# Performance work log

Measured on AMD Instinct MI355X. Metric: run time of the kernel, lower is better.

The kernel has to match this reference:

```python
import jax, jax.numpy as jnp
import numpy as np

EPS_ATTN = 1e-6
EPS_LN = 1e-5


def _layer_norm(x, g, b):
    m = jnp.mean(x, axis=-1, keepdims=True)
    v = jnp.mean((x - m) ** 2, axis=-1, keepdims=True)
    return (x - m) * jax.lax.rsqrt(v + EPS_LN) * g + b


def _linear_attention(q, k, v):
    # q,k,v: [N, L/S, H, D]; elu feature map (+1 keeps values positive)
    q = jax.nn.elu(q) + 1.0
    k = jax.nn.elu(k) + 1.0
    s_len = v.shape[1]
    v = v / s_len
    kv = jnp.einsum('nshd,nshv->nhdv', k, v)            # [N,H,D,D]
    z = 1.0 / (jnp.einsum('nlhd,nhd->nlh', q, k.sum(axis=1)) + EPS_ATTN)
    out = jnp.einsum('nlhd,nhdv->nlhv', q, kv) * z[..., None] * s_len
    return out


def setup_inputs() -> dict:
    key = jax.random.key(0)
    ks = jax.random.split(key, 8)
    N, L, S, H, D = 4, 4096, 4096, 8, 64
    sc = 0.05
    return {
        'x': jax.random.normal(ks[0], (N, L, H, D), jnp.float32),
        'source': jax.random.normal(ks[1], (N, S, H, D), jnp.float32),
        'wq': jax.random.normal(ks[2], (D, D), jnp.float32) * sc,
        'wk': jax.random.normal(ks[3], (D, D), jnp.float32) * sc,
        'wv': jax.random.normal(ks[4], (D, D), jnp.float32) * sc,
        'wmerge': jax.random.normal(ks[5], (D, D), jnp.float32) * sc,
        'w1': jax.random.normal(ks[6], (2 * D, 2 * D), jnp.float32) * sc,
        'w2': jax.random.normal(ks[7], (D, 2 * D), jnp.float32) * sc,
        'g1': jnp.ones((D,), jnp.float32),
        'b1': jnp.zeros((D,), jnp.float32),
        'g2': jnp.ones((D,), jnp.float32),
        'b2': jnp.zeros((D,), jnp.float32),
    }


def reference(x, source, wq, wk, wv, wmerge, w1, w2, g1, b1, g2, b2):
    # projections (torch Linear: y = x @ W.T), applied on last dim D=d_model
    q = jnp.einsum('nlhd,ed->nlhe', x, wq)
    k = jnp.einsum('nshd,ed->nshe', source, wk)
    v = jnp.einsum('nshd,ed->nshe', source, wv)
    message = _linear_attention(q, k, v)                # [N,L,H,D]
    message = jnp.einsum('nlhd,ed->nlhe', message, wmerge)
    message = _layer_norm(message, g1, b1)
    h = jnp.concatenate([x, message], axis=-1)          # [N,L,H,2D]
    h = jax.nn.relu(jnp.einsum('nlhd,ed->nlhe', h, w1))
    h = jnp.einsum('nlhd,ed->nlhe', h, w2)              # [N,L,H,D]
    h = _layer_norm(h, g2, b2)
    return x + h
```

## Files before the change

### kernel.cpp

```cpp
#include <hip/hip_runtime.h>
#include <cstdint>

#define NB 4
#define LL 4096
#define SS 4096
#define HH 8
#define DD 64
#define NHC (NB*HH)

typedef unsigned short ushort_t;
typedef __bf16 bf16x8 __attribute__((ext_vector_type(8)));
typedef float f32x4 __attribute__((ext_vector_type(4)));
typedef unsigned short u16x8 __attribute__((ext_vector_type(8)));

__device__ __forceinline__ float bf2f(unsigned short u) {
    union { unsigned int i; float f; } v; v.i = ((unsigned int)u) << 16; return v.f;
}
__device__ __forceinline__ unsigned short f2bf(float f) {
    union { float ff; unsigned int i; } v; v.ff = f;
    unsigned int x = v.i;
    x += 0x7fffu + ((x >> 16) & 1u);
    return (unsigned short)(x >> 16);
}
__device__ __forceinline__ bool input_is_bf16(const void* g1) {
    return ((const unsigned short*)g1)[0] == 0x3F80u;
}

template<bool BF16>
__device__ __forceinline__ float ldgf(const void* p, size_t i) {
    if constexpr (BF16) return bf2f(((const unsigned short*)p)[i]);
    else                return ((const float*)p)[i];
}
template<bool BF16>
__device__ __forceinline__ u16x8 ld8(const void* p, size_t i) {
    if constexpr (BF16) {
        return *reinterpret_cast<const u16x8*>((const unsigned short*)p + i);
    } else {
        const float* f = (const float*)p + i;
        u16x8 o;
        #pragma unroll
        for (int j = 0; j < 8; ++j) o[j] = f2bf(f[j]);
        return o;
    }
}
__device__ __forceinline__ bf16x8 ldsA(const ushort_t* p) {
    return *reinterpret_cast<const bf16x8*>(p);
}
#define MFMA16(a,b,c) __builtin_amdgcn_mfma_f32_16x16x32_bf16(a,b,c,0,0,0)

template<bool BF16, int LC>
__device__ __forceinline__ void stage_w(const void* g, size_t goff, ushort_t* dst,
                                        int rows, int dstride, int tid) {
    int total8 = (rows << LC) >> 3;
    for (int i8 = tid; i8 < total8; i8 += 256) {
        int i = i8 << 3;
        int r = i >> LC, c = i & ((1 << LC) - 1);
        *reinterpret_cast<u16x8*>(dst + r * dstride + c) = ld8<BF16>(g, goff + i);
    }
}

__device__ __forceinline__ void red16(float v[4]) {
    #pragma unroll
    for (int m = 1; m < 16; m <<= 1) {
        #pragma unroll
        for (int r = 0; r < 4; ++r) v[r] += __shfl_xor(v[r], m);
    }
}

template<bool BF16>
__device__ void kv_body(const void* __restrict__ src, const void* __restrict__ wk,
                        const void* __restrict__ wv, float* __restrict__ kvg,
                        float* __restrict__ ksumg,
                        ushort_t* S, ushort_t* KT, ushort_t* VT)
{
    const int tid = threadIdx.x;
    const int lane = tid & 63, w = tid >> 6;
    const int lg = lane >> 4, l15 = lane & 15;
    const int bid = blockIdx.x;
    const int nh = bid >> 3, ch = bid & 7;
    const int n = nh >> 3, h = nh & 7;
    const int s0 = ch * 512;
    const f32x4 z4 = {0.f, 0.f, 0.f, 0.f};

    stage_w<BF16, 6>(wk, 0, KT, 64, 136, tid);
    stage_w<BF16, 6>(wv, 0, VT, 64, 136, tid);
    __syncthreads();
    bf16x8 wkf[2][4], wvf[2][4];
    #pragma unroll
    for (int ks = 0; ks < 2; ++ks)
        #pragma unroll
        for (int nt = 0; nt < 4; ++nt) {
            wkf[ks][nt] = ldsA(KT + (nt * 16 + l15) * 136 + ks * 32 + lg * 8);
            wvf[ks][nt] = ldsA(VT + (nt * 16 + l15) * 136 + ks * 32 + lg * 8);
        }
    __syncthreads();

    f32x4 kvacc[4];
    #pragma unroll
    for (int nt = 0; nt < 4; ++nt) kvacc[nt] = z4;
    float ksp[4] = {0.f, 0.f, 0.f, 0.f};

    for (int st = 0; st < 4; ++st) {
        for (int i = tid; i < 128 * 8; i += 256) {
            int r = i >> 3, c8 = (i & 7) << 3;
            size_t gb = ((size_t)((size_t)n * SS + (s0 + st * 128 + r)) * HH + h) * DD + c8;
            *reinterpret_cast<u16x8*>(S + r * 72 + c8) = ld8<BF16>(src, gb);
        }
        __syncthreads();

        #pragma unroll
        for (int mtt = 0; mtt < 2; ++mtt) {
            const int rowA = w * 32 + mtt * 16;
            bf16x8 af[2];
            #pragma unroll
            for (int ks = 0; ks < 2; ++ks)
                af[ks] = ldsA(S + (rowA + l15) * 72 + ks * 32 + lg * 8);
            f32x4 ka[4], va[4];
            #pragma unroll
            for (int nt = 0; nt < 4; ++nt) { ka[nt] = z4; va[nt] = z4; }
            #pragma unroll
            for (int ks = 0; ks < 2; ++ks)
                #pragma unroll
                for (int nt = 0; nt < 4; ++nt) {
                    ka[nt] = MFMA16(af[ks], wkf[ks][nt], ka[nt]);
                    va[nt] = MFMA16(af[ks], wvf[ks][nt], va[nt]);
                }
            #pragma unroll
            for (int nt = 0; nt < 4; ++nt)
                #pragma unroll
                for (int r = 0; r < 4; ++r) {
                    float kvl = ka[nt][r];
                    kvl = kvl > 0.f ? kvl + 1.f : __expf(kvl);
                    ksp[nt] += kvl;
                    int srow = rowA + lg * 4 + r;
                    int dcol = nt * 16 + l15;
                    KT[dcol * 136 + srow] = f2bf(kvl);
                    VT[dcol * 136 + srow] = f2bf(va[nt][r]);
                }
        }
        __syncthreads();

        #pragma unroll
        for (int ks = 0; ks < 4; ++ks) {
            bf16x8 akv = ldsA(KT + (w * 16 + l15) * 136 + ks * 32 + lg * 8);
            #pragma unroll
            for (int nt = 0; nt < 4; ++nt) {
                bf16x8 bkv = ldsA(VT + (nt * 16 + l15) * 136 + ks * 32 + lg * 8);
                kvacc[nt] = MFMA16(akv, bkv, kvacc[nt]);
            }
        }
        __syncthreads();
    }

    float* kvo = kvg + (size_t)nh * DD * DD;
    #pragma unroll
    for (int nt = 0; nt < 4; ++nt)
        #pragma unroll
        for (int r = 0; r < 4; ++r)
            atomicAdd(&kvo[(w * 16 + lg * 4 + r) * DD + nt * 16 + l15], kvacc[nt][r]);
    #pragma unroll
    for (int m = 16; m < 64; m <<= 1)
        #pragma unroll
        for (int nt = 0; nt < 4; ++nt) ksp[nt] += __shfl_xor(ksp[nt], m);
    if (lane < 16) {
        #pragma unroll
        for (int nt = 0; nt < 4; ++nt)
            atomicAdd(&ksumg[nh * DD + nt * 16 + lane], ksp[nt]);
    }
}

__global__ __launch_bounds__(256, 2) void kv_kernel(
    const void* __restrict__ src, const void* __restrict__ wk, const void* __restrict__ wv,
    const void* __restrict__ g1, float* __restrict__ kvg, float* __restrict__ ksumg)
{
    __shared__ ushort_t S[128 * 72];
    __shared__ ushort_t KT[64 * 136];
    __shared__ ushort_t VT[64 * 136];
    if (input_is_bf16(g1)) kv_body<true >(src, wk, wv, kvg, ksumg, S, KT, VT);
    else                   kv_body<false>(src, wk, wv, kvg, ksumg, S, KT, VT);
}

template<bool BF16>
__device__ void main_body(const void* __restrict__ x,
                          const void* __restrict__ wq, const void* __restrict__ wm,
                          const void* __restrict__ w1, const void* __restrict__ w2,
                          const void* __restrict__ g1, const void* __restrict__ b1,
                          const void* __restrict__ g2, const void* __restrict__ b2,
                          const float* __restrict__ kvg, const float* __restrict__ ksumg,
                          void* __restrict__ outp,
                          ushort_t* w1s, ushort_t* kvs, ushort_t* B0, ushort_t* B1,
                          ushort_t* B2)
{
    const int tid = threadIdx.x;
    const int lane = tid & 63, w = tid >> 6;
    const int lg = lane >> 4, l15 = lane & 15;
    const int bid = blockIdx.x;
    const int nh = bid >> 4, ch = bid & 15;
    const int n = nh >> 3, h = nh & 7;
    const int rowA = w * 16;
    const f32x4 z4 = {0.f, 0.f, 0.f, 0.f};

    stage_w<BF16, 6>(wq, 0, B0, 64, 72, tid);
    stage_w<BF16, 6>(wm, 0, B1, 64, 72, tid);
    stage_w<BF16, 7>(w2, 0, w1s, 64, 136, tid);
    for (int i = tid; i < 4096; i += 256) {
        int d = i >> 6, e = i & 63;
        B2[d * 72 + e] = f2bf(kvg[(size_t)nh * 4096 + i]);
    }
    __syncthreads();

    bf16x8 wqf[2][4], w2f[4][4];
    #pragma unroll
    for (int ks = 0; ks < 2; ++ks)
        #pragma unroll
        for (int nt = 0; nt < 4; ++nt)
            wqf[ks][nt] = ldsA(B0 + (nt * 16 + l15) * 72 + ks * 32 + lg * 8);
    #pragma unroll
    for (int ks = 0; ks < 4; ++ks)
        #pragma unroll
        for (int nt = 0; nt < 4; ++nt)
            w2f[ks][nt] = ldsA(w1s + (nt * 16 + l15) * 136 + ks * 32 + lg * 8);
    {
        bf16x8 akv[2];
        #pragma unroll
        for (int ks = 0; ks < 2; ++ks)
            akv[ks] = ldsA(B2 + (w * 16 + l15) * 72 + ks * 32 + lg * 8);
        f32x4 km[4];
        #pragma unroll
        for (int nt = 0; nt < 4; ++nt) km[nt] = z4;
        #pragma unroll
        for (int ks = 0; ks < 2; ++ks)
            #pragma unroll
            for (int nt = 0; nt < 4; ++nt) {
                bf16x8 bwm = ldsA(B1 + (nt * 16 + l15) * 72 + ks * 32 + lg * 8);
                km[nt] = MFMA16(akv[ks], bwm, km[nt]);
            }
        #pragma unroll
        for (int nt = 0; nt < 4; ++nt)
            #pragma unroll
            for (int r = 0; r < 4; ++r)
                kvs[(nt * 16 + l15) * 72 + w * 16 + lg * 4 + r] = f2bf(km[nt][r]);
    }
    __syncthreads();

    stage_w<BF16, 7>(w1, 0, w1s, 128, 136, tid);
    bf16x8 kvmf[2][4];
    #pragma unroll
    for (int ks = 0; ks < 2; ++ks)
        #pragma unroll
        for (int nt = 0; nt < 4; ++nt)
            kvmf[ks][nt] = ldsA(kvs + (nt * 16 + l15) * 72 + ks * 32 + lg * 8);
    float g1r[4], b1r[4], g2r[4], b2r[4], ksr[4];
    #pragma unroll
    for (int nt = 0; nt < 4; ++nt) {
        int c = nt * 16 + l15;
        g1r[nt] = ldgf<BF16>(g1, c); b1r[nt] = ldgf<BF16>(b1, c);
        g2r[nt] = ldgf<BF16>(g2, c); b2r[nt] = ldgf<BF16>(b2, c);
        ksr[nt] = ksumg[nh * 64 + c];
    }
    __syncthreads();

    for (int t = 0; t < 4; ++t) {
        const int l0 = ch * 256 + t * 64;

        #pragma unroll
        for (int p = 0; p < 2; ++p) {
            int r16 = p * 8 + (lane >> 3), c8 = (lane & 7) << 3;
            size_t gb = ((size_t)((size_t)n * LL + (l0 + rowA + r16)) * HH + h) * DD + c8;
            *reinterpret_cast<u16x8*>(B0 + (rowA + r16) * 72 + c8) = ld8<BF16>(x, gb);
        }

        bf16x8 af[2];
        #pragma unroll
        for (int ks = 0; ks < 2; ++ks)
            af[ks] = ldsA(B0 + (rowA + l15) * 72 + ks * 32 + lg * 8);
        f32x4 qa[4];
        #pragma unroll
        for (int nt = 0; nt < 4; ++nt) qa[nt] = z4;
        #pragma unroll
        for (int ks = 0; ks < 2; ++ks)
            #pragma unroll
            for (int nt = 0; nt < 4; ++nt)
                qa[nt] = MFMA16(af[ks], wqf[ks][nt], qa[nt]);
        float zp[4] = {0.f, 0.f, 0.f, 0.f};
        #pragma unroll
        for (int nt = 0; nt < 4; ++nt)
            #pragma unroll
            for (int r = 0; r < 4; ++r) {
                float v = qa[nt][r];
                v = v > 0.f ? v + 1.f : __expf(v);
                zp[r] += v * ksr[nt];
                B1[(rowA + lg * 4 + r) * 72 + nt * 16 + l15] = f2bf(v);
            }
        red16(zp);
        float zr[4];
        #pragma unroll
        for (int r = 0; r < 4; ++r) zr[r] = 1.f / (zp[r] + 1e-6f);

        #pragma unroll
        for (int ks = 0; ks < 2; ++ks)
            af[ks] = ldsA(B1 + (rowA + l15) * 72 + ks * 32 + lg * 8);
        f32x4 ma[4];
        #pragma unroll
        for (int nt = 0; nt < 4; ++nt) ma[nt] = z4;
        #pragma unroll
        for (int ks = 0; ks < 2; ++ks)
            #pragma unroll
            for (int nt = 0; nt < 4; ++nt)
                ma[nt] = MFMA16(af[ks], kvmf[ks][nt], ma[nt]);
        #pragma unroll
        for (int nt = 0; nt < 4; ++nt)
            #pragma unroll
            for (int r = 0; r < 4; ++r) ma[nt][r] *= zr[r];

        float s1[4] = {0.f,0.f,0.f,0.f}, s2[4] = {0.f,0.f,0.f,0.f};
        #pragma unroll
        for (int nt = 0; nt < 4; ++nt)
            #pragma unroll
            for (int r = 0; r < 4; ++r) {
                float v = ma[nt][r]; s1[r] += v; s2[r] += v * v;
            }
        red16(s1); red16(s2);
        #pragma unroll
        for (int r = 0; r < 4; ++r) {
            float mu = s1[r] * 0.015625f;
            float var = s2[r] * 0.015625f - mu * mu;
            s1[r] = mu; s2[r] = rsqrtf(var + 1e-5f);
        }
        #pragma unroll
        for (int nt = 0; nt < 4; ++nt)
            #pragma unroll
            for (int r = 0; r < 4; ++r)
                B1[(rowA + lg * 4 + r) * 72 + nt * 16 + l15] =
                    f2bf((ma[nt][r] - s1[r]) * s2[r] * g1r[nt] + b1r[nt]);

        f32x4 ha[4];
        #pragma unroll
        for (int nt = 0; nt < 4; ++nt) ha[nt] = z4;
        #pragma unroll
        for (int half = 0; half < 2; ++half) {
            f32x4 ta[4];
            #pragma unroll
            for (int nt = 0; nt < 4; ++nt) ta[nt] = z4;
            #pragma unroll
            for (int ks = 0; ks < 4; ++ks) {
                const ushort_t* bp = (ks < 2) ? B0 : B1;
                bf16x8 a1 = ldsA(bp + (rowA + l15) * 72 + (ks & 1) * 32 + lg * 8);
                #pragma unroll
                for (int nt = 0; nt < 4; ++nt) {
                    bf16x8 bw = ldsA(w1s + (half * 64 + nt * 16 + l15) * 136 + ks * 32 + lg * 8);
                    ta[nt] = MFMA16(a1, bw, ta[nt]);
                }
            }
            #pragma unroll
            for (int nt = 0; nt < 4; ++nt)
                #pragma unroll
                for (int r = 0; r < 4; ++r)
                    B2[(rowA + lg * 4 + r) * 72 + nt * 16 + l15] =
                        f2bf(fmaxf(ta[nt][r], 0.f));
            #pragma unroll
            for (int k2 = 0; k2 < 2; ++k2) {
                bf16x8 a2 = ldsA(B2 + (rowA + l15) * 72 + k2 * 32 + lg * 8);
                #pragma unroll
                for (int nt = 0; nt < 4; ++nt)
                    ha[nt] = MFMA16(a2, w2f[half * 2 + k2][nt], ha[nt]);
            }
        }

        float t1[4] = {0.f,0.f,0.f,0.f}, t2[4] = {0.f,0.f,0.f,0.f};
        #pragma unroll
        for (int nt = 0; nt < 4; ++nt)
            #pragma unroll
            for (int r = 0; r < 4; ++r) {
                float v = ha[nt][r]; t1[r] += v; t2[r] += v * v;
            }
        red16(t1); red16(t2);
        #pragma unroll
        for (int r = 0; r < 4; ++r) {
            float mu = t1[r] * 0.015625f;
            float var = t2[r] * 0.015625f - mu * mu;
            t1[r] = mu; t2[r] = rsqrtf(var + 1e-5f);
        }
        #pragma unroll
        for (int nt = 0; nt < 4; ++nt)
            #pragma unroll
            for (int r = 0; r < 4; ++r) {
                float xv = bf2f(B0[(rowA + lg * 4 + r) * 72 + nt * 16 + l15]);
                float ov = xv + (ha[nt][r] - t1[r]) * t2[r] * g2r[nt] + b2r[nt];
                B1[(rowA + lg * 4 + r) * 72 + nt * 16 + l15] = f2bf(ov);
            }

        #pragma unroll
        for (int p = 0; p < 2; ++p) {
            int r16 = p * 8 + (lane >> 3), c8 = (lane & 7) << 3;
            size_t gb = ((size_t)((size_t)n * LL + (l0 + rowA + r16)) * HH + h) * DD + c8;
            u16x8 v = *reinterpret_cast<const u16x8*>(B1 + (rowA + r16) * 72 + c8);
            if constexpr (BF16) {
                *reinterpret_cast<u16x8*>((unsigned short*)outp + gb) = v;
            } else {
                float* fo = (float*)outp + gb;
                #pragma unroll
                for (int j = 0; j < 8; ++j) fo[j] = bf2f(v[j]);
            }
        }
    }
}

__global__ __launch_bounds__(256, 2) void main_kernel(
    const void* __restrict__ x,
    const void* __restrict__ wq, const void* __restrict__ wm,
    const void* __restrict__ w1, const void* __restrict__ w2,
    const void* __restrict__ g1, const void* __restrict__ b1,
    const void* __restrict__ g2, const void* __restrict__ b2,
    const float* __restrict__ kvg, const float* __restrict__ ksumg,
    void* __restrict__ outp)
{
    __shared__ ushort_t w1s[128 * 136];
    __shared__ ushort_t kvs[64 * 72];
    __shared__ ushort_t B0[64 * 72];
    __shared__ ushort_t B1[64 * 72];
    __shared__ ushort_t B2[64 * 72];
    if (input_is_bf16(g1))
        main_body<true >(x, wq, wm, w1, w2, g1, b1, g2, b2, kvg, ksumg, outp,
                         w1s, kvs, B0, B1, B2);
    else
        main_body<false>(x, wq, wm, w1, w2, g1, b1, g2, b2, kvg, ksumg, outp,
                         w1s, kvs, B0, B1, B2);
}

extern "C" void kernel_launch(void* const* d_in, const int* in_sizes, int n_in,
                              void* d_out, int out_size, void* d_ws, size_t ws_size,
                              hipStream_t stream) {
    const void* x   = d_in[0];
    const void* src = d_in[1];
    const void* wq  = d_in[2];
    const void* wk  = d_in[3];
    const void* wv  = d_in[4];
    const void* wm  = d_in[5];
    const void* w1  = d_in[6];
    const void* w2  = d_in[7];
    const void* g1  = d_in[8];
    const void* b1  = d_in[9];
    const void* g2  = d_in[10];
    const void* b2  = d_in[11];

    float* kvg   = (float*)d_ws;
    float* ksumg = kvg + (size_t)NHC * DD * DD;

    hipMemsetAsync(d_ws, 0, ((size_t)NHC * DD * DD + NHC * DD) * sizeof(float), stream);
    kv_kernel<<<NHC * 8, 256, 0, stream>>>(src, wk, wv, g1, kvg, ksumg);
    main_kernel<<<NHC * 16, 256, 0, stream>>>(x, wq, wm, w1, w2, g1, b1, g2, b2,
                                              kvg, ksumg, d_out);
}
```

Before: 165.0 us.

## Split KV reduction across more blocks, prefetch x tiles, use native bf16 convert

The KV kernel now launches four times as many blocks, each handling a single 128-row chunk with no inner loop, so more CUs run in parallel. The cost is four times as many atomicAdds into the kv and ksum accumulators. The main kernel loads the next x tile into registers while the current tile is being computed, which hides global load latency at the price of extra registers. The manual round-to-nearest bf16 conversion is replaced by the compiler's native cast.

Measured after the change: 166.7 us. No clear change (+1.0%).

```diff
diff --git a/kernel.cpp b/kernel.cpp
--- a/kernel.cpp
+++ b/kernel.cpp
@@ -17,10 +17,8 @@
     union { unsigned int i; float f; } v; v.i = ((unsigned int)u) << 16; return v.f;
 }
 __device__ __forceinline__ unsigned short f2bf(float f) {
-    union { float ff; unsigned int i; } v; v.ff = f;
-    unsigned int x = v.i;
-    x += 0x7fffu + ((x >> 16) & 1u);
-    return (unsigned short)(x >> 16);
+    __bf16 h = (__bf16)f;
+    return __builtin_bit_cast(unsigned short, h);
 }
 __device__ __forceinline__ bool input_is_bf16(const void* g1) {
     return ((const unsigned short*)g1)[0] == 0x3F80u;
@@ -77,14 +75,20 @@
     const int lane = tid & 63, w = tid >> 6;
     const int lg = lane >> 4, l15 = lane & 15;
     const int bid = blockIdx.x;
-    const int nh = bid >> 3, ch = bid & 7;
+    const int nh = bid >> 5, ch = bid & 31;
     const int n = nh >> 3, h = nh & 7;
-    const int s0 = ch * 512;
+    const int s0 = ch * 128;
     const f32x4 z4 = {0.f, 0.f, 0.f, 0.f};
 
+    for (int i = tid; i < 128 * 8; i += 256) {
+        int r = i >> 3, c8 = (i & 7) << 3;
+        size_t gb = ((size_t)((size_t)n * SS + (s0 + r)) * HH + h) * DD + c8;
+        *reinterpret_cast<u16x8*>(S + r * 72 + c8) = ld8<BF16>(src, gb);
+    }
     stage_w<BF16, 6>(wk, 0, KT, 64, 136, tid);
     stage_w<BF16, 6>(wv, 0, VT, 64, 136, tid);
     __syncthreads();
+
     bf16x8 wkf[2][4], wvf[2][4];
     #pragma unroll
     for (int ks = 0; ks < 2; ++ks)
@@ -95,61 +99,50 @@
         }
     __syncthreads();
 
+    float ksp[4] = {0.f, 0.f, 0.f, 0.f};
+    #pragma unroll
+    for (int mtt = 0; mtt < 2; ++mtt) {
+        const int rowA = w * 32 + mtt * 16;
+        bf16x8 af[2];
+        #pragma unroll
+        for (int ks = 0; ks < 2; ++ks)
+            af[ks] = ldsA(S + (rowA + l15) * 72 + ks * 32 + lg * 8);
+        f32x4 ka[4], va[4];
+        #pragma unroll
+        for (int nt = 0; nt < 4; ++nt) { ka[nt] = z4; va[nt] = z4; }
+        #pragma unroll
+        for (int ks = 0; ks < 2; ++ks)
+            #pragma unroll
+            for (int nt = 0; nt < 4; ++nt) {
+                ka[nt] = MFMA16(af[ks], wkf[ks][nt], ka[nt]);
+                va[nt] = MFMA16(af[ks], wvf[ks][nt], va[nt]);
+            }
+        #pragma unroll
+        for (int nt = 0; nt < 4; ++nt)
+            #pragma unroll
+            for (int r = 0; r < 4; ++r) {
+                float kvl = ka[nt][r];
+                kvl = kvl > 0.f ? kvl + 1.f : __expf(kvl);
+                ksp[nt] += kvl;
+                int srow = rowA + lg * 4 + r;
+                int dcol = nt * 16 + l15;
+                KT[dcol * 136 + srow] = f2bf(kvl);
+                VT[dcol * 136 + srow] = f2bf(va[nt][r]);
+            }
+    }
+    __syncthreads();
+
     f32x4 kvacc[4];
     #pragma unroll
     for (int nt = 0; nt < 4; ++nt) kvacc[nt] = z4;
-    float ksp[4] = {0.f, 0.f, 0.f, 0.f};
-
-    for (int st = 0; st < 4; ++st) {
-        for (int i = tid; i < 128 * 8; i += 256) {
-            int r = i >> 3, c8 = (i & 7) << 3;
-            size_t gb = ((size_t)((size_t)n * SS + (s0 + st * 128 + r)) * HH + h) * DD + c8;
-            *reinterpret_cast<u16x8*>(S + r * 72 + c8) = ld8<BF16>(src, gb);
-        }
-        __syncthreads();
-
-        #pragma unroll
-        for (int mtt = 0; mtt < 2; ++mtt) {
-            const int rowA = w * 32 + mtt * 16;
-            bf16x8 af[2];
-            #pragma unroll
-            for (int ks = 0; ks < 2; ++ks)
-                af[ks] = ldsA(S + (rowA + l15) * 72 + ks * 32 + lg * 8);
-            f32x4 ka[4], va[4];
-            #pragma unroll
-            for (int nt = 0; nt < 4; ++nt) { ka[nt] = z4; va[nt] = z4; }
-            #pragma unroll
-            for (int ks = 0; ks < 2; ++ks)
-                #pragma unroll
-                for (int nt = 0; nt < 4; ++nt) {
-                    ka[nt] = MFMA16(af[ks], wkf[ks][nt], ka[nt]);
-                    va[nt] = MFMA16(af[ks], wvf[ks][nt], va[nt]);
-                }
-            #pragma unroll
-            for (int nt = 0; nt < 4; ++nt)
-                #pragma unroll
-                for (int r = 0; r < 4; ++r) {
-                    float kvl = ka[nt][r];
-                    kvl = kvl > 0.f ? kvl + 1.f : __expf(kvl);
-                    ksp[nt] += kvl;
-                    int srow = rowA + lg * 4 + r;
-                    int dcol = nt * 16 + l15;
-                    KT[dcol * 136 + srow] = f2bf(kvl);
-                    VT[dcol * 136 + srow] = f2bf(va[nt][r]);
-                }
-        }
-        __syncthreads();
-
-        #pragma unroll
-        for (int ks = 0; ks < 4; ++ks) {
-            bf16x8 akv = ldsA(KT + (w * 16 + l15) * 136 + ks * 32 + lg * 8);
-            #pragma unroll
-            for (int nt = 0; nt < 4; ++nt) {
-                bf16x8 bkv = ldsA(VT + (nt * 16 + l15) * 136 + ks * 32 + lg * 8);
-                kvacc[nt] = MFMA16(akv, bkv, kvacc[nt]);
-            }
-        }
-        __syncthreads();
+    #pragma unroll
+    for (int ks = 0; ks < 4; ++ks) {
+        bf16x8 akv = ldsA(KT + (w * 16 + l15) * 136 + ks * 32 + lg * 8);
+        #pragma unroll
+        for (int nt = 0; nt < 4; ++nt) {
+            bf16x8 bkv = ldsA(VT + (nt * 16 + l15) * 136 + ks * 32 + lg * 8);
+            kvacc[nt] = MFMA16(akv, bkv, kvacc[nt]);
+        }
     }
 
     float* kvo = kvg + (size_t)nh * DD * DD;
@@ -260,14 +253,31 @@
     }
     __syncthreads();
 
+    const int pr = lane >> 3, pc8 = (lane & 7) << 3;
+    u16x8 xpre[2];
+    {
+        const int l0 = ch * 256;
+        #pragma unroll
+        for (int p = 0; p < 2; ++p) {
+            size_t gb = ((size_t)((size_t)n * LL + (l0 + rowA + p * 8 + pr)) * HH + h) * DD + pc8;
+            xpre[p] = ld8<BF16>(x, gb);
+        }
+    }
+
     for (int t = 0; t < 4; ++t) {
         const int l0 = ch * 256 + t * 64;
 
         #pragma unroll
-        for (int p = 0; p < 2; ++p) {
-            int r16 = p * 8 + (lane >> 3), c8 = (lane & 7) << 3;
-            size_t gb = ((size_t)((size_t)n * LL + (l0 + rowA + r16)) * HH + h) * DD + c8;
-            *reinterpret_cast<u16x8*>(B0 + (rowA + r16) * 72 + c8) = ld8<BF16>(x, gb);
+        for (int p = 0; p < 2; ++p)
+            *reinterpret_cast<u16x8*>(B0 + (rowA + p * 8 + pr) * 72 + pc8) = xpre[p];
+
+        u16x8 xnext[2];
+        if (t < 3) {
+            #pragma unroll
+            for (int p = 0; p < 2; ++p) {
+                size_t gb = ((size_t)((size_t)n * LL + (l0 + 64 + rowA + p * 8 + pr)) * HH + h) * DD + pc8;
+                xnext[p] = ld8<BF16>(x, gb);
+            }
         }
 
         bf16x8 af[2];
@@ -392,9 +402,8 @@
 
         #pragma unroll
         for (int p = 0; p < 2; ++p) {
-            int r16 = p * 8 + (lane >> 3), c8 = (lane & 7) << 3;
-            size_t gb = ((size_t)((size_t)n * LL + (l0 + rowA + r16)) * HH + h) * DD + c8;
-            u16x8 v = *reinterpret_cast<const u16x8*>(B1 + (rowA + r16) * 72 + c8);
+            size_t gb = ((size_t)((size_t)n * LL + (l0 + rowA + p * 8 + pr)) * HH + h) * DD + pc8;
+            u16x8 v = *reinterpret_cast<const u16x8*>(B1 + (rowA + p * 8 + pr) * 72 + pc8);
             if constexpr (BF16) {
                 *reinterpret_cast<u16x8*>((unsigned short*)outp + gb) = v;
             } else {
@@ -403,6 +412,8 @@
                 for (int j = 0; j < 8; ++j) fo[j] = bf2f(v[j]);
             }
         }
+
+        xpre[0] = xnext[0]; xpre[1] = xnext[1];
     }
 }
 
@@ -448,7 +459,7 @@
     float* ksumg = kvg + (size_t)NHC * DD * DD;
 
     hipMemsetAsync(d_ws, 0, ((size_t)NHC * DD * DD + NHC * DD) * sizeof(float), stream);
-    kv_kernel<<<NHC * 8, 256, 0, stream>>>(src, wk, wv, g1, kvg, ksumg);
+    kv_kernel<<<NHC * 32, 256, 0, stream>>>(src, wk, wv, g1, kvg, ksumg);
     main_kernel<<<NHC * 16, 256, 0, stream>>>(x, wq, wm, w1, w2, g1, b1, g2, b2,
                                               kvg, ksumg, d_out);
 }
```
